# Optimization experiments

Measured on AMD Instinct MI355X. Metric: run time of the kernel, lower is better.

Reference implementation:

```python
import jax, jax.numpy as jnp
import numpy as np

D_MODEL = 1024
NUM_HEADS = 16
HEAD_DIM = D_MODEL // NUM_HEADS


def setup_inputs() -> dict:
    key = jax.random.key(0)
    ks = jax.random.split(key, 9)
    s = 1.0 / np.sqrt(D_MODEL)
    def lin(k):
        kw, kb = jax.random.split(k)
        W = jax.random.uniform(kw, (D_MODEL, D_MODEL), jnp.float32, -s, s)
        b = jax.random.uniform(kb, (D_MODEL,), jnp.float32, -s, s)
        return W, b
    Wq, bq = lin(ks[0])
    Wk, bk = lin(ks[1])
    Wv, bv = lin(ks[2])
    Wo, bo = lin(ks[3])
    x = jax.random.normal(ks[4], (4, 2048, D_MODEL), jnp.float32)
    return {"x": x, "Wq": Wq, "bq": bq, "Wk": Wk, "bk": bk,
            "Wv": Wv, "bv": bv, "Wo": Wo, "bo": bo}


def reference(x, Wq, bq, Wk, bk, Wv, bv, Wo, bo):
    B, S, _ = x.shape
    def heads(W, b):
        # [B,S,D] -> [B,H,S,Dh]
        return (x @ W.T + b).reshape(B, S, NUM_HEADS, HEAD_DIM).transpose(0, 2, 1, 3)
    q = heads(Wq, bq)
    k = heads(Wk, bk)
    v = heads(Wv, bv)
    scale = jnp.sqrt(jnp.float32(HEAD_DIM))
    scores = jnp.einsum('bhqd,bhkd->bhqk', q, k) / scale  # [B,H,S,S]
    attn = jax.nn.softmax(scores, axis=-1)
    ctx = jnp.einsum('bhqk,bhkd->bhqd', attn, v)
    ctx = ctx.transpose(0, 2, 1, 3).reshape(B, S, D_MODEL)
    out = ctx @ Wo.T + bo
    return out
```

## Files before the change

### kernel.cpp

```cpp
#include <hip/hip_runtime.h>
#include <hip/hip_bf16.h>

typedef __bf16 bf16;
typedef __attribute__((ext_vector_type(4))) __bf16 bf16x4;
typedef __attribute__((ext_vector_type(8))) __bf16 bf16x8;
typedef __attribute__((ext_vector_type(4))) float floatx4;

#define MFMA_16x16x32(a, b, c) __builtin_amdgcn_mfma_f32_16x16x32_bf16((a), (b), (c), 0, 0, 0)

#define SOFTMAX_SC 0.18033688011112042f

__device__ __forceinline__ void async_lds16(const bf16* g, bf16* lds) {
  __builtin_amdgcn_global_load_lds(
      (__attribute__((address_space(1))) void*)(g),
      (__attribute__((address_space(3))) void*)(lds),
      16, 0, 0);
}

__global__ __launch_bounds__(256) void cast_all_kernel(
    const float* __restrict__ x,
    const float* __restrict__ Wq, const float* __restrict__ Wk,
    const float* __restrict__ Wv, const float* __restrict__ Wo,
    bf16* __restrict__ dst)
{
  const size_t xN = (size_t)8192 * 1024;
  size_t i = ((size_t)blockIdx.x * 256 + threadIdx.x) * 8;
  const float* src;
  size_t off;
  if (i < xN) { src = x; off = i; }
  else {
    size_t j = i - xN;
    int w = (int)(j >> 20);
    off = j & (((size_t)1 << 20) - 1);
    src = (w == 0) ? Wq : (w == 1) ? Wk : (w == 2) ? Wv : Wo;
  }
  floatx4 a = *(const floatx4*)(src + off);
  floatx4 b = *(const floatx4*)(src + off + 4);
  bf16x8 r;
  r[0] = (bf16)a[0]; r[1] = (bf16)a[1]; r[2] = (bf16)a[2]; r[3] = (bf16)a[3];
  r[4] = (bf16)b[0]; r[5] = (bf16)b[1]; r[6] = (bf16)b[2]; r[7] = (bf16)b[3];
  *(bf16x8*)(dst + i) = r;
}

template <typename CT>
__device__ __forceinline__ void gemm128_async_body(
    const bf16* __restrict__ A, const bf16* __restrict__ W,
    const float* __restrict__ bias, CT* __restrict__ C)
{
  __shared__ __align__(16) bf16 As[128 * 64];
  __shared__ __align__(16) bf16 Bs[128 * 64];

  const int tid  = threadIdx.x;
  const int lane = tid & 63;
  const int wave = tid >> 6;
  const int quad = lane >> 4;
  const int l15  = lane & 15;

  const int gm0   = blockIdx.y * 128;
  const int gn0   = blockIdx.x * 128;
  const int m_off = (wave >> 1) * 64;
  const int n_off = (wave & 1) * 64;

  floatx4 acc[4][4] = {};

  const bf16* ap[4];
  const bf16* wp[4];
  #pragma unroll
  for (int i = 0; i < 4; ++i) {
    int c = i * 256 + tid;
    int srow = c >> 3;
    int ksw  = (c & 7) ^ (srow & 7);
    ap[i] = A + (size_t)(gm0 + srow) * 1024 + ksw * 8;
    wp[i] = W + (size_t)(gn0 + srow) * 1024 + ksw * 8;
  }

  for (int kt = 0; kt < 16; ++kt) {
    __syncthreads();
    #pragma unroll
    for (int i = 0; i < 4; ++i) {
      int c = i * 256 + tid;
      async_lds16(ap[i], &As[c * 8]);
      async_lds16(wp[i], &Bs[c * 8]);
      ap[i] += 64; wp[i] += 64;
    }
    __syncthreads();

    #pragma unroll
    for (int kk = 0; kk < 2; ++kk) {
      bf16x8 af[4], bfr[4];
      #pragma unroll
      for (int i = 0; i < 4; ++i) {
        int rm = m_off + i * 16 + l15;
        af[i]  = *(const bf16x8*)&As[rm * 64 + (((kk * 4 + quad) ^ (rm & 7)) * 8)];
        int rn = n_off + i * 16 + l15;
        bfr[i] = *(const bf16x8*)&Bs[rn * 64 + (((kk * 4 + quad) ^ (rn & 7)) * 8)];
      }
      #pragma unroll
      for (int i = 0; i < 4; ++i)
        #pragma unroll
        for (int j = 0; j < 4; ++j)
          acc[i][j] = MFMA_16x16x32(af[i], bfr[j], acc[i][j]);
    }
  }

  #pragma unroll
  for (int j = 0; j < 4; ++j) {
    const int gcol = gn0 + n_off + j * 16 + l15;
    const float bv = bias[gcol];
    #pragma unroll
    for (int i = 0; i < 4; ++i) {
      const int gr = gm0 + m_off + i * 16 + quad * 4;
      #pragma unroll
      for (int r = 0; r < 4; ++r)
        C[(size_t)(gr + r) * 1024 + gcol] = (CT)(acc[i][j][r] + bv);
    }
  }
}

__global__ __launch_bounds__(256) void o_gemm_async(
    const bf16* __restrict__ ctx, const bf16* __restrict__ Wob,
    const float* __restrict__ bo, float* __restrict__ out)
{
  gemm128_async_body<float>(ctx, Wob, bo, out);
}

__global__ __launch_bounds__(512, 4) void qkv_gemm256(
    const bf16* __restrict__ xb,
    const bf16* __restrict__ Wqb, const float* __restrict__ bq,
    const bf16* __restrict__ Wkb, const float* __restrict__ bk,
    const bf16* __restrict__ Wvb, const float* __restrict__ bv,
    bf16* Q, bf16* K, bf16* Vt)
{
  __shared__ __align__(16) bf16 As[256 * 64];
  __shared__ __align__(16) bf16 Bs[128 * 64];

  const int z = blockIdx.z;
  const bf16* W = (z == 0) ? Wqb : (z == 1) ? Wkb : Wvb;
  const float* bias = (z == 0) ? bq : (z == 1) ? bk : bv;

  const int tid  = threadIdx.x;
  const int lane = tid & 63;
  const int wave = tid >> 6;
  const int quad = lane >> 4;
  const int l15  = lane & 15;

  const int gm0   = blockIdx.y * 256;
  const int gn0   = blockIdx.x * 128;
  const int m_off = (wave >> 1) * 64;
  const int n_off = (wave & 1) * 64;

  floatx4 acc[4][4] = {};

  const bf16* ap[4];
  const bf16* wp[2];
  #pragma unroll
  for (int i = 0; i < 4; ++i) {
    int c = i * 512 + tid;
    int srow = c >> 3;
    int ksw  = (c & 7) ^ (srow & 7);
    ap[i] = xb + (size_t)(gm0 + srow) * 1024 + ksw * 8;
  }
  #pragma unroll
  for (int i = 0; i < 2; ++i) {
    int c = i * 512 + tid;
    int srow = c >> 3;
    int ksw  = (c & 7) ^ (srow & 7);
    wp[i] = W + (size_t)(gn0 + srow) * 1024 + ksw * 8;
  }

  for (int kt = 0; kt < 16; ++kt) {
    __syncthreads();
    #pragma unroll
    for (int i = 0; i < 4; ++i) {
      async_lds16(ap[i], &As[(i * 512 + tid) * 8]);
      ap[i] += 64;
    }
    #pragma unroll
    for (int i = 0; i < 2; ++i) {
      async_lds16(wp[i], &Bs[(i * 512 + tid) * 8]);
      wp[i] += 64;
    }
    __syncthreads();

    #pragma unroll
    for (int kk = 0; kk < 2; ++kk) {
      bf16x8 af[4], bfr[4];
      #pragma unroll
      for (int i = 0; i < 4; ++i) {
        int rm = m_off + i * 16 + l15;
        af[i]  = *(const bf16x8*)&As[rm * 64 + (((kk * 4 + quad) ^ (rm & 7)) * 8)];
        int rn = n_off + i * 16 + l15;
        bfr[i] = *(const bf16x8*)&Bs[rn * 64 + (((kk * 4 + quad) ^ (rn & 7)) * 8)];
      }
      #pragma unroll
      for (int i = 0; i < 4; ++i)
        #pragma unroll
        for (int j = 0; j < 4; ++j)
          acc[i][j] = MFMA_16x16x32(af[i], bfr[j], acc[i][j]);
    }
  }

  #pragma unroll
  for (int j = 0; j < 4; ++j) {
    const int gcol = gn0 + n_off + j * 16 + l15;
    const float bv = bias[gcol];
    #pragma unroll
    for (int i = 0; i < 4; ++i) {
      const int gr = gm0 + m_off + i * 16 + quad * 4;
      if (z == 2) {
        const int h  = gcol >> 6;
        const int dh = gcol & 63;
        const size_t base =
            (((size_t)(gr >> 11) * 16 + h) * 64 + dh) * 2048 + (gr & 2047);
        bf16x4 pk;
        #pragma unroll
        for (int r = 0; r < 4; ++r) pk[r] = (bf16)(acc[i][j][r] + bv);
        *(bf16x4*)&Vt[base] = pk;
      } else {
        bf16* dst = (z == 0) ? Q : K;
        const float sc = (z == 0) ? SOFTMAX_SC : 1.0f;
        #pragma unroll
        for (int r = 0; r < 4; ++r)
          dst[(size_t)(gr + r) * 1024 + gcol] = (bf16)((acc[i][j][r] + bv) * sc);
      }
    }
  }
}

__global__ __launch_bounds__(512, 4) void flash7_kernel(
    const bf16* __restrict__ Q, const bf16* __restrict__ Kg,
    const bf16* __restrict__ Vtg, bf16* __restrict__ ctx)
{
  __shared__ __align__(16) bf16 Ks[2][64 * 64];
  __shared__ __align__(16) bf16 Vts[2][64 * 64];
  __shared__ __align__(16) bf16 Ps[8 * 32 * 72];

  const int tid  = threadIdx.x;
  const int lane = tid & 63;
  const int wave = tid >> 6;
  const int quad = lane >> 4;
  const int l15  = lane & 15;

  const int bh = blockIdx.y;
  const int b  = bh >> 4;
  const int h  = bh & 15;
  const int qt = blockIdx.x;

  const size_t row0 = (size_t)b * 2048;
  const int col0 = h * 64;

  const int qbase = qt * 256 + wave * 32;
  bf16x8 qf[2][2];
  #pragma unroll
  for (int q = 0; q < 2; ++q) {
    const bf16* qp = Q + (row0 + qbase + q * 16 + l15) * 1024 + col0 + quad * 8;
    qf[q][0] = *(const bf16x8*)(qp);
    qf[q][1] = *(const bf16x8*)(qp + 32);
  }

  floatx4 o_acc[2][4] = {};
  float l_sum[2] = {0.0f, 0.0f};

  const int srow = tid >> 3;
  const int cell = (tid & 7) ^ (srow & 7);
  const bf16* kp = Kg + (row0 + srow) * 1024 + col0 + cell * 8;
  const bf16* vp = Vtg + ((size_t)bh * 64 + srow) * 2048 + cell * 8;
  const int soff = tid * 8;

  async_lds16(kp, &Ks[0][soff]);
  async_lds16(vp, &Vts[0][soff]);
  kp += 64 * 1024;
  vp += 64;

  bf16* const ps_base = &Ps[(wave * 32 + l15) * 72];

  for (int kb = 0; kb < 32; ++kb) {
    const int cur = kb & 1;
    const bf16* const Kc = Ks[cur];
    const bf16* const Vc = Vts[cur];

    __syncthreads();

    if (kb < 31) {
      async_lds16(kp, &Ks[cur ^ 1][soff]);
      async_lds16(vp, &Vts[cur ^ 1][soff]);
      kp += 64 * 1024;
      vp += 64;
    }

    #pragma unroll
    for (int j = 0; j < 4; ++j) {
      const int rk = j * 16 + l15;
      bf16x8 k0 = *(const bf16x8*)&Kc[rk * 64 + ((quad ^ (rk & 7)) * 8)];
      bf16x8 k1 = *(const bf16x8*)&Kc[rk * 64 + (((4 + quad) ^ (rk & 7)) * 8)];
      #pragma unroll
      for (int q = 0; q < 2; ++q) {
        floatx4 z = {};
        z = MFMA_16x16x32(k0, qf[q][0], z);
        z = MFMA_16x16x32(k1, qf[q][1], z);
        bf16x4 pk;
        #pragma unroll
        for (int r = 0; r < 4; ++r) {
          float p = exp2f(z[r]);
          z[r] = p;
          pk[r] = (bf16)p;
        }
        l_sum[q] += (z[0] + z[1]) + (z[2] + z[3]);
        *(bf16x4*)(ps_base + q * (16 * 72) + j * 16 + quad * 4) = pk;
      }
    }

    #pragma unroll
    for (int kk = 0; kk < 2; ++kk) {
      bf16x8 vf[4];
      #pragma unroll
      for (int t = 0; t < 4; ++t) {
        const int rd = t * 16 + l15;
        vf[t] = *(const bf16x8*)&Vc[rd * 64 + (((kk * 4 + quad) ^ (rd & 7)) * 8)];
      }
      bf16x8 pf0 = *(const bf16x8*)(ps_base + kk * 32 + quad * 8);
      bf16x8 pf1 = *(const bf16x8*)(ps_base + 16 * 72 + kk * 32 + quad * 8);
      __builtin_amdgcn_s_setprio(1);
      #pragma unroll
      for (int t = 0; t < 4; ++t) {
        o_acc[0][t] = MFMA_16x16x32(pf0, vf[t], o_acc[0][t]);
        o_acc[1][t] = MFMA_16x16x32(pf1, vf[t], o_acc[1][t]);
      }
      __builtin_amdgcn_s_setprio(0);
    }
  }

  #pragma unroll
  for (int q = 0; q < 2; ++q) {
    l_sum[q] += __shfl_xor(l_sum[q], 16, 64);
    l_sum[q] += __shfl_xor(l_sum[q], 32, 64);
  }
  #pragma unroll
  for (int q = 0; q < 2; ++q) {
    float li[4];
    #pragma unroll
    for (int r = 0; r < 4; ++r)
      li[r] = 1.0f / __shfl(l_sum[q], quad * 4 + r, 64);
    #pragma unroll
    for (int t = 0; t < 4; ++t) {
      const int gc = col0 + t * 16 + l15;
      #pragma unroll
      for (int r = 0; r < 4; ++r) {
        const int srow2 = qbase + q * 16 + quad * 4 + r;
        ctx[(row0 + srow2) * 1024 + gc] = (bf16)(o_acc[q][t][r] * li[r]);
      }
    }
  }
}

__device__ __forceinline__ bf16x8 load8(const bf16* p) { return *(const bf16x8*)p; }
__device__ __forceinline__ bf16x8 load8(const float* p) {
  floatx4 a = *(const floatx4*)p;
  floatx4 b = *(const floatx4*)(p + 4);
  bf16x8 r;
  r[0] = (bf16)a[0]; r[1] = (bf16)a[1]; r[2] = (bf16)a[2]; r[3] = (bf16)a[3];
  r[4] = (bf16)b[0]; r[5] = (bf16)b[1]; r[6] = (bf16)b[2]; r[7] = (bf16)b[3];
  return r;
}

template <typename AT, typename CT>
__device__ __forceinline__ void gemm128_body_fb(
    const AT* __restrict__ A, const float* __restrict__ W,
    const float* __restrict__ bias, CT* __restrict__ C)
{
  constexpr int LDP = 72;
  __shared__ __align__(16) bf16 As[128 * LDP];
  __shared__ __align__(16) bf16 Bs[128 * LDP];
  const int tid = threadIdx.x, lane = tid & 63, wave = tid >> 6;
  const int quad = lane >> 4, l15 = lane & 15;
  const int gm0 = blockIdx.y * 128, gn0 = blockIdx.x * 128;
  const int m_off = (wave >> 1) * 64, n_off = (wave & 1) * 64;
  floatx4 acc[4][4] = {};
  int srow[4], scol[4];
  #pragma unroll
  for (int i = 0; i < 4; ++i) {
    int c = i * 256 + tid;
    srow[i] = c >> 3; scol[i] = (c & 7) * 8;
  }
  for (int kt = 0; kt < 16; ++kt) {
    bf16x8 ar[4], br[4];
    #pragma unroll
    for (int i = 0; i < 4; ++i) {
      ar[i] = load8(A + (size_t)(gm0 + srow[i]) * 1024 + kt * 64 + scol[i]);
      br[i] = load8(W + (size_t)(gn0 + srow[i]) * 1024 + kt * 64 + scol[i]);
    }
    __syncthreads();
    #pragma unroll
    for (int i = 0; i < 4; ++i) {
      *(bf16x8*)&As[srow[i] * LDP + scol[i]] = ar[i];
      *(bf16x8*)&Bs[srow[i] * LDP + scol[i]] = br[i];
    }
    __syncthreads();
    #pragma unroll
    for (int kk = 0; kk < 2; ++kk) {
      bf16x8 af[4], bfr[4];
      #pragma unroll
      for (int i = 0; i < 4; ++i) {
        af[i]  = *(const bf16x8*)&As[(m_off + i * 16 + l15) * LDP + (kk * 4 + quad) * 8];
        bfr[i] = *(const bf16x8*)&Bs[(n_off + i * 16 + l15) * LDP + (kk * 4 + quad) * 8];
      }
      #pragma unroll
      for (int i = 0; i < 4; ++i)
        #pragma unroll
        for (int j = 0; j < 4; ++j)
          acc[i][j] = MFMA_16x16x32(af[i], bfr[j], acc[i][j]);
    }
  }
  #pragma unroll
  for (int j = 0; j < 4; ++j) {
    const int gcol = gn0 + n_off + j * 16 + l15;
    const float bv = bias[gcol];
    #pragma unroll
    for (int i = 0; i < 4; ++i) {
      const int gr = gm0 + m_off + i * 16 + quad * 4;
      #pragma unroll
      for (int r = 0; r < 4; ++r)
        C[(size_t)(gr + r) * 1024 + gcol] = (CT)(acc[i][j][r] + bv);
    }
  }
}

__global__ __launch_bounds__(256) void qkv_gemm_fb(
    const float* __restrict__ x,
    const float* __restrict__ Wq, const float* __restrict__ bq,
    const float* __restrict__ Wk, const float* __restrict__ bk,
    const float* __restrict__ Wv, const float* __restrict__ bv,
    bf16* Q, bf16* K, bf16* V)
{
  const float* W; const float* bias; bf16* out;
  if (blockIdx.z == 0)      { W = Wq; bias = bq; out = Q; }
  else if (blockIdx.z == 1) { W = Wk; bias = bk; out = K; }
  else                      { W = Wv; bias = bv; out = V; }
  gemm128_body_fb<float, bf16>(x, W, bias, out);
}

__global__ __launch_bounds__(256) void out_gemm_fb(
    const bf16* __restrict__ ctx, const float* __restrict__ Wo,
    const float* __restrict__ bo, float* __restrict__ out)
{
  gemm128_body_fb<bf16, float>(ctx, Wo, bo, out);
}

__global__ __launch_bounds__(512) void flash_fb(
    const bf16* Q, const bf16* __restrict__ Kg, const bf16* __restrict__ Vg,
    bf16* ctx)
{
  __shared__ __align__(16) bf16 Ks[64 * 72];
  __shared__ __align__(16) bf16 Vs[64 * 72];
  __shared__ __align__(16) bf16 Vt[64 * 72];
  __shared__ __align__(16) bf16 Ps[8 * 16 * 72];
  const int tid = threadIdx.x, lane = tid & 63, wave = tid >> 6;
  const int quad = lane >> 4, l15 = lane & 15;
  const int bh = blockIdx.y, b = bh >> 4, h = bh & 15, qt = blockIdx.x;
  const size_t row0 = (size_t)b * 2048;
  const int col0 = h * 64;
  const int qs = qt * 128 + wave * 16 + l15;
  const bf16* qp = Q + (row0 + qs) * 1024 + col0 + quad * 8;
  const bf16x8 qf0 = *(const bf16x8*)(qp);
  const bf16x8 qf1 = *(const bf16x8*)(qp + 32);
  floatx4 o_acc[4] = {};
  float l_part[4] = {0.0f, 0.0f, 0.0f, 0.0f};
  const float SC = SOFTMAX_SC;
  const int srow = tid >> 3, scol = (tid & 7) * 8;
  const bf16* kptr = Kg + (row0 + srow) * 1024 + col0 + scol;
  const bf16* vptr = Vg + (row0 + srow) * 1024 + col0 + scol;
  const int td = tid & 63, tg = tid >> 6;
  for (int kb = 0; kb < 32; ++kb) {
    bf16x8 kr = *(const bf16x8*)kptr;
    bf16x8 vr = *(const bf16x8*)vptr;
    kptr += 64 * 1024; vptr += 64 * 1024;
    __syncthreads();
    *(bf16x8*)&Ks[srow * 72 + scol] = kr;
    *(bf16x8*)&Vs[srow * 72 + scol] = vr;
    __syncthreads();
    {
      bf16x8 t;
      #pragma unroll
      for (int j = 0; j < 8; ++j) t[j] = Vs[(tg * 8 + j) * 72 + td];
      *(bf16x8*)&Vt[td * 72 + tg * 8] = t;
    }
    floatx4 sc[4];
    #pragma unroll
    for (int j = 0; j < 4; ++j) {
      int rk = j * 16 + l15;
      bf16x8 k0 = *(const bf16x8*)&Ks[rk * 72 + quad * 8];
      bf16x8 k1 = *(const bf16x8*)&Ks[rk * 72 + 32 + quad * 8];
      floatx4 z = {};
      z = MFMA_16x16x32(qf0, k0, z);
      z = MFMA_16x16x32(qf1, k1, z);
      sc[j] = z;
    }
    #pragma unroll
    for (int j = 0; j < 4; ++j)
      #pragma unroll
      for (int r = 0; r < 4; ++r) {
        float p = exp2f(fminf(sc[j][r] * SC, 60.0f));
        sc[j][r] = p;
        l_part[r] += p;
      }
    #pragma unroll
    for (int j = 0; j < 4; ++j)
      #pragma unroll
      for (int r = 0; r < 4; ++r)
        Ps[(wave * 16 + quad * 4 + r) * 72 + j * 16 + l15] = (bf16)sc[j][r];
    __syncthreads();
    #pragma unroll
    for (int kk = 0; kk < 2; ++kk) {
      bf16x8 pf = *(const bf16x8*)&Ps[(wave * 16 + l15) * 72 + kk * 32 + quad * 8];
      #pragma unroll
      for (int t = 0; t < 4; ++t) {
        bf16x8 vf = *(const bf16x8*)&Vt[(t * 16 + l15) * 72 + kk * 32 + quad * 8];
        o_acc[t] = MFMA_16x16x32(pf, vf, o_acc[t]);
      }
    }
  }
  #pragma unroll
  for (int off = 1; off < 16; off <<= 1)
    #pragma unroll
    for (int r = 0; r < 4; ++r)
      l_part[r] += __shfl_xor(l_part[r], off, 64);
  #pragma unroll
  for (int r = 0; r < 4; ++r) l_part[r] = 1.0f / l_part[r];
  #pragma unroll
  for (int t = 0; t < 4; ++t)
    #pragma unroll
    for (int r = 0; r < 4; ++r) {
      int srow2 = qt * 128 + wave * 16 + quad * 4 + r;
      ctx[(row0 + srow2) * 1024 + col0 + t * 16 + l15] = (bf16)(o_acc[t][r] * l_part[r]);
    }
}

extern "C" void kernel_launch(void* const* d_in, const int* in_sizes, int n_in,
                              void* d_out, int out_size, void* d_ws, size_t ws_size,
                              hipStream_t stream) {
  (void)in_sizes; (void)n_in; (void)out_size;
  const float* x  = (const float*)d_in[0];
  const float* Wq = (const float*)d_in[1];
  const float* bq = (const float*)d_in[2];
  const float* Wk = (const float*)d_in[3];
  const float* bk = (const float*)d_in[4];
  const float* Wv = (const float*)d_in[5];
  const float* bv = (const float*)d_in[6];
  const float* Wo = (const float*)d_in[7];
  const float* bo = (const float*)d_in[8];
  float* out = (float*)d_out;

  const size_t nE = (size_t)8192 * 1024;
  const size_t wE = (size_t)1024 * 1024;
  const size_t need = (5 * nE + 4 * wE) * sizeof(bf16);

  if (ws_size >= need) {
    bf16* Qw   = (bf16*)d_ws;
    bf16* Kw   = Qw + nE;
    bf16* Vtw  = Kw + nE;
    bf16* ctxw = Vtw + nE;
    bf16* xb   = ctxw + nE;
    bf16* Wqb  = xb + nE;
    bf16* Wkb  = Wqb + wE;
    bf16* Wvb  = Wkb + wE;
    bf16* Wob  = Wvb + wE;

    cast_all_kernel<<<dim3(6144), 256, 0, stream>>>(x, Wq, Wk, Wv, Wo, xb);

    qkv_gemm256<<<dim3(8, 32, 3), 512, 0, stream>>>(
        xb, Wqb, bq, Wkb, bk, Wvb, bv, Qw, Kw, Vtw);
    flash7_kernel<<<dim3(8, 64), 512, 0, stream>>>(Qw, Kw, Vtw, ctxw);
    o_gemm_async<<<dim3(8, 64), 256, 0, stream>>>(ctxw, Wob, bo, out);
  } else {
    bf16* Qw = (bf16*)d_ws;
    bf16* Kw = Qw + nE;
    bf16* Vw = Kw + nE;
    bf16* ctx = (ws_size >= 4 * nE * sizeof(bf16)) ? (Vw + nE) : Qw;
    qkv_gemm_fb<<<dim3(8, 64, 3), 256, 0, stream>>>(x, Wq, bq, Wk, bk, Wv, bv, Qw, Kw, Vw);
    flash_fb<<<dim3(16, 64), 512, 0, stream>>>(Qw, Kw, Vw, ctx);
    out_gemm_fb<<<dim3(8, 64), 256, 0, stream>>>(ctx, Wo, bo, out);
  }
}
```

Measured before the change: 307.8 us.

## Halve flash query tile, pass P via ds_bpermute, remap blocks

The flash attention kernel now gives each wave 16 query rows instead of 32, so each 512-thread block covers 128 queries and the grid grows to 16x64. The softmax probabilities move from the score layout to the MFMA A-operand layout through ds_bpermute cross-lane shuffles instead of being staged in a shared-memory P buffer, which removes that LDS array. Launch bounds are raised to allow more resident blocks per CU, and the block index is remapped to interleave heads and query tiles across XCDs. In exchange, each K/V tile loaded into LDS is reused by half as many queries, so total K/V traffic doubles.

```diff
diff --git a/kernel.cpp b/kernel.cpp
--- a/kernel.cpp
+++ b/kernel.cpp
@@ -2,9 +2,11 @@
 #include <hip/hip_bf16.h>
 
 typedef __bf16 bf16;
+typedef __attribute__((ext_vector_type(2))) __bf16 bf16x2;
 typedef __attribute__((ext_vector_type(4))) __bf16 bf16x4;
 typedef __attribute__((ext_vector_type(8))) __bf16 bf16x8;
 typedef __attribute__((ext_vector_type(4))) float floatx4;
+typedef __attribute__((ext_vector_type(4))) int intx4;
 
 #define MFMA_16x16x32(a, b, c) __builtin_amdgcn_mfma_f32_16x16x32_bf16((a), (b), (c), 0, 0, 0)
 
@@ -227,13 +229,12 @@
   }
 }
 
-__global__ __launch_bounds__(512, 4) void flash7_kernel(
+__global__ __launch_bounds__(512, 6) void flash8_kernel(
     const bf16* __restrict__ Q, const bf16* __restrict__ Kg,
     const bf16* __restrict__ Vtg, bf16* __restrict__ ctx)
 {
   __shared__ __align__(16) bf16 Ks[2][64 * 64];
   __shared__ __align__(16) bf16 Vts[2][64 * 64];
-  __shared__ __align__(16) bf16 Ps[8 * 32 * 72];
 
   const int tid  = threadIdx.x;
   const int lane = tid & 63;
@@ -241,25 +242,23 @@
   const int quad = lane >> 4;
   const int l15  = lane & 15;
 
-  const int bh = blockIdx.y;
+  int bid = blockIdx.y * 16 + blockIdx.x;
+  bid = (bid & 7) * 128 + (bid >> 3);
+  const int qt = bid & 15;
+  const int bh = bid >> 4;
   const int b  = bh >> 4;
   const int h  = bh & 15;
-  const int qt = blockIdx.x;
 
   const size_t row0 = (size_t)b * 2048;
   const int col0 = h * 64;
 
-  const int qbase = qt * 256 + wave * 32;
-  bf16x8 qf[2][2];
-  #pragma unroll
-  for (int q = 0; q < 2; ++q) {
-    const bf16* qp = Q + (row0 + qbase + q * 16 + l15) * 1024 + col0 + quad * 8;
-    qf[q][0] = *(const bf16x8*)(qp);
-    qf[q][1] = *(const bf16x8*)(qp + 32);
-  }
-
-  floatx4 o_acc[2][4] = {};
-  float l_sum[2] = {0.0f, 0.0f};
+  const int qbase = qt * 128 + wave * 16;
+  const bf16* qp = Q + (row0 + qbase + l15) * 1024 + col0 + quad * 8;
+  const bf16x8 qf0 = *(const bf16x8*)(qp);
+  const bf16x8 qf1 = *(const bf16x8*)(qp + 32);
+
+  floatx4 o_acc[4] = {};
+  float l_sum = 0.0f;
 
   const int srow = tid >> 3;
   const int cell = (tid & 7) ^ (srow & 7);
@@ -272,7 +271,8 @@
   kp += 64 * 1024;
   vp += 64;
 
-  bf16* const ps_base = &Ps[(wave * 32 + l15) * 72];
+  const int addr0 = (2 * (quad & 1)) * 64 + l15 * 4;
+  const int addr1 = addr0 + 64;
 
   for (int kb = 0; kb < 32; ++kb) {
     const int cur = kb & 1;
@@ -288,25 +288,35 @@
       vp += 64;
     }
 
+    unsigned int pw[4][2];
     #pragma unroll
     for (int j = 0; j < 4; ++j) {
       const int rk = j * 16 + l15;
       bf16x8 k0 = *(const bf16x8*)&Kc[rk * 64 + ((quad ^ (rk & 7)) * 8)];
       bf16x8 k1 = *(const bf16x8*)&Kc[rk * 64 + (((4 + quad) ^ (rk & 7)) * 8)];
-      #pragma unroll
-      for (int q = 0; q < 2; ++q) {
-        floatx4 z = {};
-        z = MFMA_16x16x32(k0, qf[q][0], z);
-        z = MFMA_16x16x32(k1, qf[q][1], z);
-        bf16x4 pk;
-        #pragma unroll
-        for (int r = 0; r < 4; ++r) {
-          float p = exp2f(z[r]);
-          z[r] = p;
-          pk[r] = (bf16)p;
-        }
-        l_sum[q] += (z[0] + z[1]) + (z[2] + z[3]);
-        *(bf16x4*)(ps_base + q * (16 * 72) + j * 16 + quad * 4) = pk;
+      floatx4 z = {};
+      z = MFMA_16x16x32(k0, qf0, z);
+      z = MFMA_16x16x32(k1, qf1, z);
+      const float e0 = exp2f(z[0]);
+      const float e1 = exp2f(z[1]);
+      const float e2 = exp2f(z[2]);
+      const float e3 = exp2f(z[3]);
+      l_sum += (e0 + e1) + (e2 + e3);
+      bf16x2 t0; t0[0] = (bf16)e0; t0[1] = (bf16)e1;
+      bf16x2 t1; t1[0] = (bf16)e2; t1[1] = (bf16)e3;
+      pw[j][0] = __builtin_bit_cast(unsigned int, t0);
+      pw[j][1] = __builtin_bit_cast(unsigned int, t1);
+    }
+
+    int pa[2][4];
+    #pragma unroll
+    for (int f = 0; f < 2; ++f) {
+      #pragma unroll
+      for (int w = 0; w < 4; ++w) {
+        const int a = (w >> 1) ? addr1 : addr0;
+        const int lo = __builtin_amdgcn_ds_bpermute(a, (int)pw[2 * f][w & 1]);
+        const int hi = __builtin_amdgcn_ds_bpermute(a, (int)pw[2 * f + 1][w & 1]);
+        pa[f][w] = (quad >= 2) ? hi : lo;
       }
     }
 
@@ -318,37 +328,30 @@
         const int rd = t * 16 + l15;
         vf[t] = *(const bf16x8*)&Vc[rd * 64 + (((kk * 4 + quad) ^ (rd & 7)) * 8)];
       }
-      bf16x8 pf0 = *(const bf16x8*)(ps_base + kk * 32 + quad * 8);
-      bf16x8 pf1 = *(const bf16x8*)(ps_base + 16 * 72 + kk * 32 + quad * 8);
+      intx4 pv;
+      pv[0] = pa[kk][0]; pv[1] = pa[kk][1]; pv[2] = pa[kk][2]; pv[3] = pa[kk][3];
+      const bf16x8 pf = __builtin_bit_cast(bf16x8, pv);
       __builtin_amdgcn_s_setprio(1);
       #pragma unroll
-      for (int t = 0; t < 4; ++t) {
-        o_acc[0][t] = MFMA_16x16x32(pf0, vf[t], o_acc[0][t]);
-        o_acc[1][t] = MFMA_16x16x32(pf1, vf[t], o_acc[1][t]);
-      }
+      for (int t = 0; t < 4; ++t)
+        o_acc[t] = MFMA_16x16x32(pf, vf[t], o_acc[t]);
       __builtin_amdgcn_s_setprio(0);
     }
   }
 
-  #pragma unroll
-  for (int q = 0; q < 2; ++q) {
-    l_sum[q] += __shfl_xor(l_sum[q], 16, 64);
-    l_sum[q] += __shfl_xor(l_sum[q], 32, 64);
-  }
-  #pragma unroll
-  for (int q = 0; q < 2; ++q) {
-    float li[4];
-    #pragma unroll
-    for (int r = 0; r < 4; ++r)
-      li[r] = 1.0f / __shfl(l_sum[q], quad * 4 + r, 64);
-    #pragma unroll
-    for (int t = 0; t < 4; ++t) {
-      const int gc = col0 + t * 16 + l15;
-      #pragma unroll
-      for (int r = 0; r < 4; ++r) {
-        const int srow2 = qbase + q * 16 + quad * 4 + r;
-        ctx[(row0 + srow2) * 1024 + gc] = (bf16)(o_acc[q][t][r] * li[r]);
-      }
+  l_sum += __shfl_xor(l_sum, 16, 64);
+  l_sum += __shfl_xor(l_sum, 32, 64);
+  float li[4];
+  #pragma unroll
+  for (int r = 0; r < 4; ++r)
+    li[r] = 1.0f / __shfl(l_sum, quad * 4 + r, 64);
+  #pragma unroll
+  for (int t = 0; t < 4; ++t) {
+    const int gc = col0 + t * 16 + l15;
+    #pragma unroll
+    for (int r = 0; r < 4; ++r) {
+      const int srow2 = qbase + quad * 4 + r;
+      ctx[(row0 + srow2) * 1024 + gc] = (bf16)(o_acc[t][r] * li[r]);
     }
   }
 }
@@ -569,7 +572,7 @@
 
     qkv_gemm256<<<dim3(8, 32, 3), 512, 0, stream>>>(
         xb, Wqb, bq, Wkb, bk, Wvb, bv, Qw, Kw, Vtw);
-    flash7_kernel<<<dim3(8, 64), 512, 0, stream>>>(Qw, Kw, Vtw, ctxw);
+    flash8_kernel<<<dim3(16, 64), 512, 0, stream>>>(Qw, Kw, Vtw, ctxw);
     o_gemm_async<<<dim3(8, 64), 256, 0, stream>>>(ctxw, Wob, bo, out);
   } else {
     bf16* Qw = (bf16*)d_ws;
```

Result: no change. 312.4 us (+1.5%).

## Remap blocks across XCDs, compute softmax row sums via MFMA, swizzle P LDS

Applied to the files above, without the earlier changes.

Block indices for the QKV GEMM, the attention kernel and the output GEMM are remapped so that consecutive hardware block IDs, which are dealt round-robin across the 8 XCDs, land on related tiles. The intent is better L2 reuse of shared K/V and weight tiles. In the attention kernel the per-lane softmax denominator accumulation and its end-of-loop shuffles are replaced by an extra MFMA of P against a ones vector, and LDS offsets are precomputed. The P staging buffer gets an XOR swizzle to reduce bank conflicts, at the cost of splitting each P read into two 8-byte loads and adding extra MFMA work.

```diff
diff --git a/kernel.cpp b/kernel.cpp
--- a/kernel.cpp
+++ b/kernel.cpp
@@ -2,6 +2,7 @@
 #include <hip/hip_bf16.h>
 
 typedef __bf16 bf16;
+typedef __attribute__((ext_vector_type(2))) __bf16 bf16x2;
 typedef __attribute__((ext_vector_type(4))) __bf16 bf16x4;
 typedef __attribute__((ext_vector_type(8))) __bf16 bf16x8;
 typedef __attribute__((ext_vector_type(4))) float floatx4;
@@ -45,7 +46,8 @@
 template <typename CT>
 __device__ __forceinline__ void gemm128_async_body(
     const bf16* __restrict__ A, const bf16* __restrict__ W,
-    const float* __restrict__ bias, CT* __restrict__ C)
+    const float* __restrict__ bias, CT* __restrict__ C,
+    int gm0, int gn0)
 {
   __shared__ __align__(16) bf16 As[128 * 64];
   __shared__ __align__(16) bf16 Bs[128 * 64];
@@ -56,8 +58,6 @@
   const int quad = lane >> 4;
   const int l15  = lane & 15;
 
-  const int gm0   = blockIdx.y * 128;
-  const int gn0   = blockIdx.x * 128;
   const int m_off = (wave >> 1) * 64;
   const int n_off = (wave & 1) * 64;
 
@@ -121,7 +121,9 @@
     const bf16* __restrict__ ctx, const bf16* __restrict__ Wob,
     const float* __restrict__ bo, float* __restrict__ out)
 {
-  gemm128_async_body<float>(ctx, Wob, bo, out);
+  const int flat = blockIdx.y * 8 + blockIdx.x;
+  const int L = (flat & 7) * 64 + (flat >> 3);
+  gemm128_async_body<float>(ctx, Wob, bo, out, (L >> 3) * 128, (L & 7) * 128);
 }
 
 __global__ __launch_bounds__(512, 4) void qkv_gemm256(
@@ -134,7 +136,12 @@
   __shared__ __align__(16) bf16 As[256 * 64];
   __shared__ __align__(16) bf16 Bs[128 * 64];
 
-  const int z = blockIdx.z;
+  const int flat = blockIdx.x + 8 * (blockIdx.y + 32 * blockIdx.z);
+  const int L = (flat & 7) * 96 + (flat >> 3);
+  const int z  = L >> 8;
+  const int gy = (L >> 3) & 31;
+  const int gx = L & 7;
+
   const bf16* W = (z == 0) ? Wqb : (z == 1) ? Wkb : Wvb;
   const float* bias = (z == 0) ? bq : (z == 1) ? bk : bv;
 
@@ -144,8 +151,8 @@
   const int quad = lane >> 4;
   const int l15  = lane & 15;
 
-  const int gm0   = blockIdx.y * 256;
-  const int gn0   = blockIdx.x * 128;
+  const int gm0   = gy * 256;
+  const int gn0   = gx * 128;
   const int m_off = (wave >> 1) * 64;
   const int n_off = (wave & 1) * 64;
 
@@ -227,7 +234,7 @@
   }
 }
 
-__global__ __launch_bounds__(512, 4) void flash7_kernel(
+__global__ __launch_bounds__(512, 4) void flash9_kernel(
     const bf16* __restrict__ Q, const bf16* __restrict__ Kg,
     const bf16* __restrict__ Vtg, bf16* __restrict__ ctx)
 {
@@ -241,10 +248,12 @@
   const int quad = lane >> 4;
   const int l15  = lane & 15;
 
-  const int bh = blockIdx.y;
+  const int flat = blockIdx.y * 8 + blockIdx.x;
+  const int L = (flat & 7) * 64 + (flat >> 3);
+  const int qt = L & 7;
+  const int bh = L >> 3;
   const int b  = bh >> 4;
   const int h  = bh & 15;
-  const int qt = blockIdx.x;
 
   const size_t row0 = (size_t)b * 2048;
   const int col0 = h * 64;
@@ -259,7 +268,11 @@
   }
 
   floatx4 o_acc[2][4] = {};
-  float l_sum[2] = {0.0f, 0.0f};
+  floatx4 l_acc[2] = {};
+
+  bf16x8 onesf;
+  #pragma unroll
+  for (int i = 0; i < 8; ++i) onesf[i] = (bf16)1.0f;
 
   const int srow = tid >> 3;
   const int cell = (tid & 7) ^ (srow & 7);
@@ -272,7 +285,35 @@
   kp += 64 * 1024;
   vp += 64;
 
-  bf16* const ps_base = &Ps[(wave * 32 + l15) * 72];
+  int koffA[4], koffB[4], vOff[2][4];
+  #pragma unroll
+  for (int j = 0; j < 4; ++j) {
+    const int rk = j * 16 + l15;
+    koffA[j] = rk * 64 + ((quad ^ (rk & 7)) * 8);
+    koffB[j] = rk * 64 + (((4 + quad) ^ (rk & 7)) * 8);
+  }
+  #pragma unroll
+  for (int kk = 0; kk < 2; ++kk)
+    #pragma unroll
+    for (int t = 0; t < 4; ++t) {
+      const int rd = t * 16 + l15;
+      vOff[kk][t] = rd * 64 + (((kk * 4 + quad) ^ (rd & 7)) * 8);
+    }
+  int pw_off[2][4];
+  #pragma unroll
+  for (int q = 0; q < 2; ++q)
+    #pragma unroll
+    for (int j = 0; j < 4; ++j)
+      pw_off[q][j] = (wave * 32 + q * 16 + l15) * 72 + (((4 * j + quad) ^ l15) * 4);
+  int pr_off[2][2][2];
+  #pragma unroll
+  for (int q = 0; q < 2; ++q)
+    #pragma unroll
+    for (int kk = 0; kk < 2; ++kk)
+      #pragma unroll
+      for (int i2 = 0; i2 < 2; ++i2)
+        pr_off[q][kk][i2] =
+            (wave * 32 + q * 16 + l15) * 72 + (((8 * kk + 2 * quad + i2) ^ l15) * 4);
 
   for (int kb = 0; kb < 32; ++kb) {
     const int cur = kb & 1;
@@ -290,9 +331,8 @@
 
     #pragma unroll
     for (int j = 0; j < 4; ++j) {
-      const int rk = j * 16 + l15;
-      bf16x8 k0 = *(const bf16x8*)&Kc[rk * 64 + ((quad ^ (rk & 7)) * 8)];
-      bf16x8 k1 = *(const bf16x8*)&Kc[rk * 64 + (((4 + quad) ^ (rk & 7)) * 8)];
+      bf16x8 k0 = *(const bf16x8*)&Kc[koffA[j]];
+      bf16x8 k1 = *(const bf16x8*)&Kc[koffB[j]];
       #pragma unroll
       for (int q = 0; q < 2; ++q) {
         floatx4 z = {};
@@ -300,13 +340,8 @@
         z = MFMA_16x16x32(k1, qf[q][1], z);
         bf16x4 pk;
         #pragma unroll
-        for (int r = 0; r < 4; ++r) {
-          float p = exp2f(z[r]);
-          z[r] = p;
-          pk[r] = (bf16)p;
-        }
-        l_sum[q] += (z[0] + z[1]) + (z[2] + z[3]);
-        *(bf16x4*)(ps_base + q * (16 * 72) + j * 16 + quad * 4) = pk;
+        for (int r = 0; r < 4; ++r) pk[r] = (bf16)exp2f(z[r]);
+        *(bf16x4*)&Ps[pw_off[q][j]] = pk;
       }
     }
 
@@ -314,33 +349,32 @@
     for (int kk = 0; kk < 2; ++kk) {
       bf16x8 vf[4];
       #pragma unroll
+      for (int t = 0; t < 4; ++t) vf[t] = *(const bf16x8*)&Vc[vOff[kk][t]];
+      bf16x8 pf[2];
+      #pragma unroll
+      for (int q = 0; q < 2; ++q) {
+        bf16x4 pa = *(const bf16x4*)&Ps[pr_off[q][kk][0]];
+        bf16x4 pb = *(const bf16x4*)&Ps[pr_off[q][kk][1]];
+        #pragma unroll
+        for (int e = 0; e < 4; ++e) { pf[q][e] = pa[e]; pf[q][e + 4] = pb[e]; }
+      }
+      __builtin_amdgcn_s_setprio(1);
+      #pragma unroll
       for (int t = 0; t < 4; ++t) {
-        const int rd = t * 16 + l15;
-        vf[t] = *(const bf16x8*)&Vc[rd * 64 + (((kk * 4 + quad) ^ (rd & 7)) * 8)];
-      }
-      bf16x8 pf0 = *(const bf16x8*)(ps_base + kk * 32 + quad * 8);
-      bf16x8 pf1 = *(const bf16x8*)(ps_base + 16 * 72 + kk * 32 + quad * 8);
-      __builtin_amdgcn_s_setprio(1);
-      #pragma unroll
-      for (int t = 0; t < 4; ++t) {
-        o_acc[0][t] = MFMA_16x16x32(pf0, vf[t], o_acc[0][t]);
-        o_acc[1][t] = MFMA_16x16x32(pf1, vf[t], o_acc[1][t]);
-      }
+        o_acc[0][t] = MFMA_16x16x32(pf[0], vf[t], o_acc[0][t]);
+        o_acc[1][t] = MFMA_16x16x32(pf[1], vf[t], o_acc[1][t]);
+      }
+      l_acc[0] = MFMA_16x16x32(pf[0], onesf, l_acc[0]);
+      l_acc[1] = MFMA_16x16x32(pf[1], onesf, l_acc[1]);
       __builtin_amdgcn_s_setprio(0);
     }
   }
 
   #pragma unroll
   for (int q = 0; q < 2; ++q) {
-    l_sum[q] += __shfl_xor(l_sum[q], 16, 64);
-    l_sum[q] += __shfl_xor(l_sum[q], 32, 64);
-  }
-  #pragma unroll
-  for (int q = 0; q < 2; ++q) {
-    float li[4];
-    #pragma unroll
-    for (int r = 0; r < 4; ++r)
-      li[r] = 1.0f / __shfl(l_sum[q], quad * 4 + r, 64);
+    floatx4 li;
+    #pragma unroll
+    for (int r = 0; r < 4; ++r) li[r] = 1.0f / l_acc[q][r];
     #pragma unroll
     for (int t = 0; t < 4; ++t) {
       const int gc = col0 + t * 16 + l15;
@@ -569,7 +603,7 @@
 
     qkv_gemm256<<<dim3(8, 32, 3), 512, 0, stream>>>(
         xb, Wqb, bq, Wkb, bk, Wvb, bv, Qw, Kw, Vtw);
-    flash7_kernel<<<dim3(8, 64), 512, 0, stream>>>(Qw, Kw, Vtw, ctxw);
+    flash9_kernel<<<dim3(8, 64), 512, 0, stream>>>(Qw, Kw, Vtw, ctxw);
     o_gemm_async<<<dim3(8, 64), 256, 0, stream>>>(ctxw, Wob, bo, out);
   } else {
     bf16* Qw = (bf16*)d_ws;
```

Result: faster. 290.6 us (-5.6%).
